# Kernel tuning notes

Hardware: AMD Instinct MI355X
Metric: run time of the kernel (lower is better)

## Reference

```python
import jax, jax.numpy as jnp
import numpy as np
import math

B, CIN, H, W = 4, 256, 64, 64
COUT = 64
K = 7  # out_kernel


def setup_inputs() -> dict:
    key = jax.random.key(0)
    ks = jax.random.split(key, 9)
    s = 0.05
    x = jax.random.normal(ks[0], (B, CIN, H, W), dtype=jnp.float32)
    Wq = jax.random.normal(ks[1], (COUT, CIN), dtype=jnp.float32) * s
    bq = jax.random.normal(ks[2], (COUT,), dtype=jnp.float32) * s
    Wk = jax.random.normal(ks[3], (COUT, CIN), dtype=jnp.float32) * s
    bk = jax.random.normal(ks[4], (COUT,), dtype=jnp.float32) * s
    Wv = jax.random.normal(ks[5], (COUT, CIN), dtype=jnp.float32) * s
    bv = jax.random.normal(ks[6], (COUT,), dtype=jnp.float32) * s
    Wout = jax.random.normal(ks[7], (COUT, COUT, K, K), dtype=jnp.float32) * s
    bout = jax.random.normal(ks[8], (COUT,), dtype=jnp.float32) * s
    return {"x": x, "Wq": Wq, "bq": bq, "Wk": Wk, "bk": bk,
            "Wv": Wv, "bv": bv, "Wout": Wout, "bout": bout}


def reference(x, Wq, bq, Wk, bk, Wv, bv, Wout, bout):
    b, c, h, w = x.shape
    C = Wq.shape[0]
    hw = h * w
    # 1x1 convs -> (b, h, w, C) channels-last
    qs = jnp.einsum('bchw,oc->bhwo', x, Wq) + bq
    ksp = jnp.einsum('bchw,oc->bhwo', x, Wk) + bk
    vs = jnp.einsum('bchw,oc->bhwo', x, Wv) + bv
    # full QK^T attention over all h*w positions
    qk = jnp.einsum('bic,bjc->bij',
                    qs.reshape(b, hw, C), ksp.reshape(b, hw, C)) / math.sqrt(float(C))
    diag = jnp.arange(hw)
    qk = qk.at[:, diag, diag].set(0.0)  # diagonal zeroed BEFORE softmax
    attn = jax.nn.softmax(qk, axis=-1).reshape(b, h, w, h, w)
    # clamped local-window indices (offsets -K//2 .. K//2)
    off = jnp.arange(K) - K // 2
    idx_h = jnp.clip(jnp.arange(h)[:, None] + off[None, :], 0, h - 1)  # (h,K)
    idx_w = jnp.clip(jnp.arange(w)[:, None] + off[None, :], 0, w - 1)  # (w,K)
    # gather attention weights at local neighborhood: (b,h,w,K,K)
    g = jnp.take_along_axis(attn, idx_h[None, :, None, :, None], axis=3)  # (b,h,w,K,w)
    g = jnp.take_along_axis(g, idx_w[None, None, :, None, :], axis=4)     # (b,h,w,K,K)
    # gather V at local neighborhood: (b,h,w,K,K,C)
    vn = vs[:, idx_h]            # (b,h,K,w,C)
    vn = vn[:, :, :, idx_w]      # (b,h,K,w,K,C)
    vn = jnp.transpose(vn, (0, 1, 3, 2, 4, 5))  # (b,h,w,K,K,C)
    # KxK stride-K conv over the (K,K) window == full contraction per pixel
    out = jnp.einsum('bhwij,bhwijc,ocij->bhwo', g, vn, Wout) + bout
    out = jax.nn.relu(out)
    return jnp.transpose(out, (0, 3, 1, 2))  # (b, C, h, w)
```

## Files before the change

### kernel.cpp

```cpp
#include <hip/hip_runtime.h>
#include <hip/hip_bf16.h>
#include <math.h>

#define BATCH 4
#define CIN   256
#define HH    64
#define WW    64
#define HW    4096
#define COUT  64
#define KK    7
#define NTAP  49
#define NSEG  16

#define QSCALE 0.18033688011112042f

typedef __attribute__((ext_vector_type(8))) short bf16x8;
typedef __attribute__((ext_vector_type(4))) float f32x4;
typedef __attribute__((ext_vector_type(4))) unsigned short u16x4;

__global__ void prep_kernel(
    const float* __restrict__ Wq, const float* __restrict__ bq,
    const float* __restrict__ Wk, const float* __restrict__ bk,
    const float* __restrict__ Wv, const float* __restrict__ bv,
    const float* __restrict__ Wout,
    __hip_bfloat16* __restrict__ Wb192, float* __restrict__ bias192,
    __hip_bfloat16* __restrict__ W2b)
{
    const int idx = blockIdx.x * 256 + threadIdx.x;
    if (idx < 192 * 256) {
        const int row = idx >> 8, c = idx & 255;
        float wsrc;
        if (row < 64)       wsrc = Wq[row * 256 + c];
        else if (row < 128) wsrc = Wk[(row - 64) * 256 + c];
        else                wsrc = Wv[(row - 128) * 256 + c];
        Wb192[idx] = __float2bfloat16(wsrc);
        if (c == 0) {
            float bsrc;
            if (row < 64)       bsrc = bq[row];
            else if (row < 128) bsrc = bk[row - 64];
            else                bsrc = bv[row - 128];
            bias192[row] = bsrc;
        }
    } else if (idx < 192 * 256 + COUT * NTAP * COUT) {
        const int j = idx - 192 * 256;
        const int o = j / (NTAP * COUT);
        const int r = j - o * (NTAP * COUT);
        const int t = r >> 6;
        const int c = r & 63;
        W2b[j] = __float2bfloat16(Wout[((size_t)o * COUT + c) * NTAP + t]);
    }
}

__global__ __launch_bounds__(256) void qkv_mfma(
    const float* __restrict__ x,
    const __hip_bfloat16* __restrict__ Wb192, const float* __restrict__ bias192,
    float* __restrict__ v,
    __hip_bfloat16* __restrict__ qh, __hip_bfloat16* __restrict__ kh)
{
    const int blk = blockIdx.x;
    const int b   = blk >> 8;
    const int p0  = (blk & 255) * 16;
    const int tid = threadIdx.x;
    const int wv  = tid >> 6;
    const int l   = tid & 63;
    const int lg  = l >> 4, lr = l & 15;

    __shared__ __attribute__((aligned(16))) __hip_bfloat16 xsh[16 * 256];

    {
        const int c0 = tid >> 2;
        const int p4 = tid & 3;
        const float4* xb4 = (const float4*)(x + ((size_t)b * CIN) * HW + p0);
#pragma unroll
        for (int it = 0; it < 4; ++it) {
            const int cc = c0 + it * 64;
            const float4 xv = xb4[(size_t)cc * (HW / 4) + p4];
            __hip_bfloat16* dst = &xsh[((cc >> 3) * 16) * 8 + (cc & 7)];
            dst[(p4 * 4 + 0) * 8] = __float2bfloat16(xv.x);
            dst[(p4 * 4 + 1) * 8] = __float2bfloat16(xv.y);
            dst[(p4 * 4 + 2) * 8] = __float2bfloat16(xv.z);
            dst[(p4 * 4 + 3) * 8] = __float2bfloat16(xv.w);
        }
    }
    __syncthreads();

    f32x4 acc0 = {0.f,0.f,0.f,0.f}, acc1 = {0.f,0.f,0.f,0.f}, acc2 = {0.f,0.f,0.f,0.f};
    const short* wb  = (const short*)Wb192;
    const short* xs  = (const short*)xsh;

#pragma unroll
    for (int s = 0; s < 8; ++s) {
        const bf16x8 af = *(const bf16x8*)(xs + (size_t)(((s * 4 + lg) * 16 + lr)) * 8);
        const bf16x8 b0 = *(const bf16x8*)(wb + (size_t)((wv * 3 + 0) * 16 + lr) * 256 + s * 32 + lg * 8);
        const bf16x8 b1 = *(const bf16x8*)(wb + (size_t)((wv * 3 + 1) * 16 + lr) * 256 + s * 32 + lg * 8);
        const bf16x8 b2 = *(const bf16x8*)(wb + (size_t)((wv * 3 + 2) * 16 + lr) * 256 + s * 32 + lg * 8);
        acc0 = __builtin_amdgcn_mfma_f32_16x16x32_bf16(af, b0, acc0, 0, 0, 0);
        acc1 = __builtin_amdgcn_mfma_f32_16x16x32_bf16(af, b1, acc1, 0, 0, 0);
        acc2 = __builtin_amdgcn_mfma_f32_16x16x32_bf16(af, b2, acc2, 0, 0, 0);
    }

    f32x4 accs[3] = {acc0, acc1, acc2};
#pragma unroll
    for (int i = 0; i < 3; ++i) {
        const int otile = wv * 3 + i;
        const int kind  = otile >> 2;
        const int o     = (otile & 3) * 16 + lr;
        const float bias = bias192[otile * 16 + lr];
#pragma unroll
        for (int j = 0; j < 4; ++j) {
            const int p = p0 + lg * 4 + j;
            const size_t addr = ((size_t)b * HW + p) * (size_t)COUT + o;
            const float val = accs[i][j] + bias;
            if (kind == 0)      { qh[addr] = __float2bfloat16(val * QSCALE); }
            else if (kind == 1) { kh[addr] = __float2bfloat16(val); }
            else                { v[addr] = val; }
        }
    }
}

__global__ __launch_bounds__(256) void qk_stats_mfma(
    const __hip_bfloat16* __restrict__ qh, const __hip_bfloat16* __restrict__ kh,
    float* __restrict__ s_part)
{
    const int blk   = blockIdx.x;
    const int b     = blk >> 8;
    const int panel = (blk >> 4) & 15;
    const int jseg  = blk & 15;
    const int tid   = threadIdx.x;
    const int w     = tid >> 6;
    const int l     = tid & 63;
    const int lg    = l >> 4;
    const int lr    = l & 15;
    const int R0    = panel * 256 + w * 64;

    const short* qb = (const short*)(qh + ((size_t)b * HW) * COUT);
    const short* kb = (const short*)(kh + ((size_t)b * HW) * COUT);

    bf16x8 a[4][2];
#pragma unroll
    for (int rt = 0; rt < 4; ++rt) {
        a[rt][0] = *(const bf16x8*)(qb + (size_t)(R0 + rt * 16 + lr) * COUT + lg * 8);
        a[rt][1] = *(const bf16x8*)(qb + (size_t)(R0 + rt * 16 + lr) * COUT + 32 + lg * 8);
    }

    float s[4][4];
#pragma unroll
    for (int rt = 0; rt < 4; ++rt)
#pragma unroll
        for (int i = 0; i < 4; ++i) s[rt][i] = 0.f;

    const int j0 = jseg * 256;
    const short* kptr = kb + (size_t)(j0 + lr) * COUT + lg * 8;

    bf16x8 p0 = *(const bf16x8*)(kptr);
    bf16x8 p1 = *(const bf16x8*)(kptr + 32);
    kptr += 16 * COUT;

    for (int it = 0; it < 16; ++it) {
        bf16x8 n0, n1;
        if (it != 15) {
            n0 = *(const bf16x8*)(kptr);
            n1 = *(const bf16x8*)(kptr + 32);
            kptr += 16 * COUT;
        }
        const int jb = j0 + it * 16;
#pragma unroll
        for (int rt = 0; rt < 4; ++rt) {
            f32x4 d = {0.f, 0.f, 0.f, 0.f};
            d = __builtin_amdgcn_mfma_f32_16x16x32_bf16(a[rt][0], p0, d, 0, 0, 0);
            d = __builtin_amdgcn_mfma_f32_16x16x32_bf16(a[rt][1], p1, d, 0, 0, 0);
            if (jb == R0 + rt * 16) {
                d.x = (lr == lg * 4 + 0) ? 0.f : d.x;
                d.y = (lr == lg * 4 + 1) ? 0.f : d.y;
                d.z = (lr == lg * 4 + 2) ? 0.f : d.z;
                d.w = (lr == lg * 4 + 3) ? 0.f : d.w;
            }
            s[rt][0] += exp2f(d.x);
            s[rt][1] += exp2f(d.y);
            s[rt][2] += exp2f(d.z);
            s[rt][3] += exp2f(d.w);
        }
        p0 = n0; p1 = n1;
    }

#pragma unroll
    for (int rt = 0; rt < 4; ++rt) {
#pragma unroll
        for (int off = 1; off < 16; off <<= 1) {
            s[rt][0] += __shfl_xor(s[rt][0], off, 64);
            s[rt][1] += __shfl_xor(s[rt][1], off, 64);
            s[rt][2] += __shfl_xor(s[rt][2], off, 64);
            s[rt][3] += __shfl_xor(s[rt][3], off, 64);
        }
        if (lr == 0) {
            float4 res = {s[rt][0], s[rt][1], s[rt][2], s[rt][3]};
            *(float4*)(s_part + (size_t)jseg * (BATCH * HW) + (size_t)b * HW +
                       R0 + rt * 16 + lg * 4) = res;
        }
    }
}

__global__ __launch_bounds__(256) void gcalc_mfma(
    const __hip_bfloat16* __restrict__ qh, const __hip_bfloat16* __restrict__ kh,
    const float* __restrict__ s_part, float* __restrict__ g)
{
    const int blk = blockIdx.x;
    const int dh  = blk % 7;
    const int bh  = blk / 7;
    const int h   = bh & 63;
    const int b   = bh >> 6;
    const int tid = threadIdx.x;
    const int wv  = tid >> 6;
    const int l   = tid & 63;
    const int lg  = l >> 4, lr = l & 15;

    const int jh = min(max(h + dh - 3, 0), HH - 1);

    __shared__ float Dsh[64][65];
    __shared__ float rsh[64];

    if (tid < 64) {
        float s = 0.f;
        const size_t base = (size_t)b * HW + h * 64 + tid;
#pragma unroll
        for (int seg = 0; seg < NSEG; ++seg)
            s += s_part[(size_t)seg * (BATCH * HW) + base];
        rsh[tid] = 1.0f / s;
    }

    const short* qb = (const short*)(qh + ((size_t)b * HW + h * 64) * COUT);
    const short* kb = (const short*)(kh + ((size_t)b * HW + jh * 64) * COUT);

    const bf16x8 a0 = *(const bf16x8*)(qb + (size_t)(wv * 16 + lr) * COUT + lg * 8);
    const bf16x8 a1 = *(const bf16x8*)(qb + (size_t)(wv * 16 + lr) * COUT + 32 + lg * 8);

#pragma unroll
    for (int ct = 0; ct < 4; ++ct) {
        const bf16x8 b0 = *(const bf16x8*)(kb + (size_t)(ct * 16 + lr) * COUT + lg * 8);
        const bf16x8 b1 = *(const bf16x8*)(kb + (size_t)(ct * 16 + lr) * COUT + 32 + lg * 8);
        f32x4 d = {0.f, 0.f, 0.f, 0.f};
        d = __builtin_amdgcn_mfma_f32_16x16x32_bf16(a0, b0, d, 0, 0, 0);
        d = __builtin_amdgcn_mfma_f32_16x16x32_bf16(a1, b1, d, 0, 0, 0);
        const int row = wv * 16 + lg * 4;
        const int col = ct * 16 + lr;
        Dsh[row + 0][col] = d.x;
        Dsh[row + 1][col] = d.y;
        Dsh[row + 2][col] = d.z;
        Dsh[row + 3][col] = d.w;
    }
    __syncthreads();

    for (int e = tid; e < 64 * 7; e += 256) {
        const int w  = e / 7;
        const int tj = e - w * 7;
        const int jw = min(max(w + tj - 3, 0), WW - 1);
        const float num = (jh == h && jw == w) ? 1.0f : exp2f(Dsh[w][jw]);
        g[((size_t)b * HW + h * 64 + w) * NTAP + dh * 7 + tj] = num * rsh[w];
    }
}

__global__ __launch_bounds__(256) void out_mfma(
    const float* __restrict__ g, const float* __restrict__ v,
    const __hip_bfloat16* __restrict__ W2b, const float* __restrict__ bout,
    float* __restrict__ out)
{
    const int blk = blockIdx.x;
    const int b   = blk >> 7;
    const int h   = (blk >> 1) & 63;
    const int w0  = (blk & 1) * 32;
    const int tid = threadIdx.x;
    const int wv  = tid >> 6;
    const int l   = tid & 63;
    const int lg  = l >> 4, lr = l & 15;

    __shared__ __attribute__((aligned(16))) __hip_bfloat16 gvsh[2][32][72];
    __shared__ float gsh[32][NTAP];

    const int row0 = b * HW + h * 64 + w0;
    for (int i = tid; i < 32 * NTAP; i += 256) {
        const int w = i / NTAP, t = i - w * NTAP;
        gsh[w][t] = g[(size_t)(row0 + w) * NTAP + t];
    }

    f32x4 acc0 = {0.f, 0.f, 0.f, 0.f};
    f32x4 acc1 = {0.f, 0.f, 0.f, 0.f};
    const float4* vb = (const float4*)(v + ((size_t)b * HW) * COUT);
    const short* wb  = (const short*)W2b + (size_t)(wv * 16 + lr) * (NTAP * COUT);

    const int fw = tid >> 4;
    const int fc4 = tid & 15;

    __syncthreads();

    for (int t = 0; t < NTAP; ++t) {
        const int dh = t / 7 - 3, dw = t - (t / 7) * 7 - 3;
        const int jh = min(max(h + dh, 0), HH - 1);
        __hip_bfloat16* dstbuf = &gvsh[t & 1][0][0];
#pragma unroll
        for (int rep = 0; rep < 2; ++rep) {
            const int w  = fw + rep * 16;
            const int jw = min(max(w0 + w + dw, 0), WW - 1);
            const float4 vvv = vb[(size_t)((jh << 6) + jw) * 16 + fc4];
            const float gg = gsh[w][t];
            u16x4 pk;
            pk.x = __builtin_bit_cast(unsigned short, __float2bfloat16(vvv.x * gg));
            pk.y = __builtin_bit_cast(unsigned short, __float2bfloat16(vvv.y * gg));
            pk.z = __builtin_bit_cast(unsigned short, __float2bfloat16(vvv.z * gg));
            pk.w = __builtin_bit_cast(unsigned short, __float2bfloat16(vvv.w * gg));
            *(u16x4*)(dstbuf + w * 72 + fc4 * 4) = pk;
        }
        const bf16x8 b0 = *(const bf16x8*)(wb + t * 64 + lg * 8);
        const bf16x8 b1 = *(const bf16x8*)(wb + t * 64 + 32 + lg * 8);
        __syncthreads();
        const short* gsrc = (const short*)&gvsh[t & 1][0][0];
        const bf16x8 a00 = *(const bf16x8*)(gsrc + (size_t)lr * 72 + lg * 8);
        const bf16x8 a01 = *(const bf16x8*)(gsrc + (size_t)lr * 72 + 32 + lg * 8);
        const bf16x8 a10 = *(const bf16x8*)(gsrc + (size_t)(16 + lr) * 72 + lg * 8);
        const bf16x8 a11 = *(const bf16x8*)(gsrc + (size_t)(16 + lr) * 72 + 32 + lg * 8);
        acc0 = __builtin_amdgcn_mfma_f32_16x16x32_bf16(a00, b0, acc0, 0, 0, 0);
        acc0 = __builtin_amdgcn_mfma_f32_16x16x32_bf16(a01, b1, acc0, 0, 0, 0);
        acc1 = __builtin_amdgcn_mfma_f32_16x16x32_bf16(a10, b0, acc1, 0, 0, 0);
        acc1 = __builtin_amdgcn_mfma_f32_16x16x32_bf16(a11, b1, acc1, 0, 0, 0);
    }

    const int o  = wv * 16 + lr;
    const float bo = bout[o];
    float* obase = out + ((size_t)(b * COUT + o) * HW) + h * 64 + w0 + lg * 4;
    float4 r0, r1;
    r0.x = fmaxf(acc0.x + bo, 0.f); r0.y = fmaxf(acc0.y + bo, 0.f);
    r0.z = fmaxf(acc0.z + bo, 0.f); r0.w = fmaxf(acc0.w + bo, 0.f);
    r1.x = fmaxf(acc1.x + bo, 0.f); r1.y = fmaxf(acc1.y + bo, 0.f);
    r1.z = fmaxf(acc1.z + bo, 0.f); r1.w = fmaxf(acc1.w + bo, 0.f);
    *(float4*)obase        = r0;
    *(float4*)(obase + 16) = r1;
}

extern "C" void kernel_launch(void* const* d_in, const int* in_sizes, int n_in,
                              void* d_out, int out_size, void* d_ws, size_t ws_size,
                              hipStream_t stream)
{
    const float* x    = (const float*)d_in[0];
    const float* Wq   = (const float*)d_in[1];
    const float* bq   = (const float*)d_in[2];
    const float* Wk   = (const float*)d_in[3];
    const float* bk   = (const float*)d_in[4];
    const float* Wv   = (const float*)d_in[5];
    const float* bv   = (const float*)d_in[6];
    const float* Wout = (const float*)d_in[7];
    const float* bout = (const float*)d_in[8];
    float* out = (float*)d_out;

    float* ws      = (float*)d_ws;
    float* v       = ws;
    float* s_part  = v + (size_t)BATCH * HW * COUT;
    float* g       = s_part + (size_t)NSEG * BATCH * HW;
    float* bias192 = g + (size_t)BATCH * HW * NTAP;
    __hip_bfloat16* qh    = (__hip_bfloat16*)(bias192 + 256);
    __hip_bfloat16* kh    = qh + (size_t)BATCH * HW * COUT;
    __hip_bfloat16* W2b   = kh + (size_t)BATCH * HW * COUT;
    __hip_bfloat16* Wb192 = W2b + (size_t)COUT * NTAP * COUT;

    prep_kernel<<<(192 * 256 + COUT * NTAP * COUT + 255) / 256, 256, 0, stream>>>(
        Wq, bq, Wk, bk, Wv, bv, Wout, Wb192, bias192, W2b);
    qkv_mfma<<<BATCH * (HW / 16), 256, 0, stream>>>(x, Wb192, bias192, v, qh, kh);
    qk_stats_mfma<<<BATCH * 16 * NSEG, 256, 0, stream>>>(qh, kh, s_part);
    gcalc_mfma<<<BATCH * HH * 7, 256, 0, stream>>>(qh, kh, s_part, g);
    out_mfma<<<512, 256, 0, stream>>>(g, v, W2b, bout, out);
}
```

Before: 183.5 us.

## Split out_mfma taps across waves and reduce partial accumulators in LDS

Restructures the output-conv kernel so that each of the four waves handles a disjoint subset of the 49 taps for all 64 output channels, instead of every wave covering all taps for 16 channels. Each wave now builds its A fragments (g-scaled V in bf16) directly in registers from global memory. This removes the per-tap shared-memory staging buffer and the per-tap __syncthreads. The partial accumulators are then summed across waves through an LDS buffer before bias and ReLU. In exchange the kernel needs more accumulator registers, more redundant global loads of V (each lane loads 8 floats per slice), and extra LDS for the final reduction.

```diff
diff --git a/kernel.cpp b/kernel.cpp
--- a/kernel.cpp
+++ b/kernel.cpp
@@ -273,66 +273,91 @@
     const int l   = tid & 63;
     const int lg  = l >> 4, lr = l & 15;
 
-    __shared__ __attribute__((aligned(16))) __hip_bfloat16 gvsh[2][32][72];
     __shared__ float gsh[32][NTAP];
+    __shared__ __attribute__((aligned(16))) float accsh[4][64][36];
 
     const int row0 = b * HW + h * 64 + w0;
     for (int i = tid; i < 32 * NTAP; i += 256) {
         const int w = i / NTAP, t = i - w * NTAP;
         gsh[w][t] = g[(size_t)(row0 + w) * NTAP + t];
     }
-
-    f32x4 acc0 = {0.f, 0.f, 0.f, 0.f};
-    f32x4 acc1 = {0.f, 0.f, 0.f, 0.f};
-    const float4* vb = (const float4*)(v + ((size_t)b * HW) * COUT);
-    const short* wb  = (const short*)W2b + (size_t)(wv * 16 + lr) * (NTAP * COUT);
-
-    const int fw = tid >> 4;
-    const int fc4 = tid & 15;
-
     __syncthreads();
 
-    for (int t = 0; t < NTAP; ++t) {
+    f32x4 acc[2][4];
+#pragma unroll
+    for (int rep = 0; rep < 2; ++rep)
+#pragma unroll
+        for (int ot = 0; ot < 4; ++ot)
+            acc[rep][ot] = (f32x4){0.f, 0.f, 0.f, 0.f};
+
+    const float* vb = v + ((size_t)b * HW) * COUT;
+    const short* wbase = (const short*)W2b;
+
+    for (int t = wv; t < NTAP; t += 4) {
         const int dh = t / 7 - 3, dw = t - (t / 7) * 7 - 3;
         const int jh = min(max(h + dh, 0), HH - 1);
-        __hip_bfloat16* dstbuf = &gvsh[t & 1][0][0];
+
+        bf16x8 A[2][2];
 #pragma unroll
         for (int rep = 0; rep < 2; ++rep) {
-            const int w  = fw + rep * 16;
+            const int w  = rep * 16 + lr;
             const int jw = min(max(w0 + w + dw, 0), WW - 1);
-            const float4 vvv = vb[(size_t)((jh << 6) + jw) * 16 + fc4];
             const float gg = gsh[w][t];
-            u16x4 pk;
-            pk.x = __builtin_bit_cast(unsigned short, __float2bfloat16(vvv.x * gg));
-            pk.y = __builtin_bit_cast(unsigned short, __float2bfloat16(vvv.y * gg));
-            pk.z = __builtin_bit_cast(unsigned short, __float2bfloat16(vvv.z * gg));
-            pk.w = __builtin_bit_cast(unsigned short, __float2bfloat16(vvv.w * gg));
-            *(u16x4*)(dstbuf + w * 72 + fc4 * 4) = pk;
-        }
-        const bf16x8 b0 = *(const bf16x8*)(wb + t * 64 + lg * 8);
-        const bf16x8 b1 = *(const bf16x8*)(wb + t * 64 + 32 + lg * 8);
-        __syncthreads();
-        const short* gsrc = (const short*)&gvsh[t & 1][0][0];
-        const bf16x8 a00 = *(const bf16x8*)(gsrc + (size_t)lr * 72 + lg * 8);
-        const bf16x8 a01 = *(const bf16x8*)(gsrc + (size_t)lr * 72 + 32 + lg * 8);
-        const bf16x8 a10 = *(const bf16x8*)(gsrc + (size_t)(16 + lr) * 72 + lg * 8);
-        const bf16x8 a11 = *(const bf16x8*)(gsrc + (size_t)(16 + lr) * 72 + 32 + lg * 8);
-        acc0 = __builtin_amdgcn_mfma_f32_16x16x32_bf16(a00, b0, acc0, 0, 0, 0);
-        acc0 = __builtin_amdgcn_mfma_f32_16x16x32_bf16(a01, b1, acc0, 0, 0, 0);
-        acc1 = __builtin_amdgcn_mfma_f32_16x16x32_bf16(a10, b0, acc1, 0, 0, 0);
-        acc1 = __builtin_amdgcn_mfma_f32_16x16x32_bf16(a11, b1, acc1, 0, 0, 0);
-    }
-
-    const int o  = wv * 16 + lr;
+            const float* vr = vb + (size_t)((jh << 6) + jw) * COUT;
+#pragma unroll
+            for (int sl = 0; sl < 2; ++sl) {
+                const float4 lo = *(const float4*)(vr + sl * 32 + lg * 8);
+                const float4 hi = *(const float4*)(vr + sl * 32 + lg * 8 + 4);
+                bf16x8 av;
+                av[0] = (short)__builtin_bit_cast(unsigned short, __float2bfloat16(lo.x * gg));
+                av[1] = (short)__builtin_bit_cast(unsigned short, __float2bfloat16(lo.y * gg));
+                av[2] = (short)__builtin_bit_cast(unsigned short, __float2bfloat16(lo.z * gg));
+                av[3] = (short)__builtin_bit_cast(unsigned short, __float2bfloat16(lo.w * gg));
+                av[4] = (short)__builtin_bit_cast(unsigned short, __float2bfloat16(hi.x * gg));
+                av[5] = (short)__builtin_bit_cast(unsigned short, __float2bfloat16(hi.y * gg));
+                av[6] = (short)__builtin_bit_cast(unsigned short, __float2bfloat16(hi.z * gg));
+                av[7] = (short)__builtin_bit_cast(unsigned short, __float2bfloat16(hi.w * gg));
+                A[rep][sl] = av;
+            }
+        }
+
+#pragma unroll
+        for (int ot = 0; ot < 4; ++ot) {
+            const short* wrow = wbase + (size_t)(ot * 16 + lr) * (NTAP * COUT) + t * 64;
+            const bf16x8 B0 = *(const bf16x8*)(wrow + lg * 8);
+            const bf16x8 B1 = *(const bf16x8*)(wrow + 32 + lg * 8);
+            acc[0][ot] = __builtin_amdgcn_mfma_f32_16x16x32_bf16(A[0][0], B0, acc[0][ot], 0, 0, 0);
+            acc[0][ot] = __builtin_amdgcn_mfma_f32_16x16x32_bf16(A[0][1], B1, acc[0][ot], 0, 0, 0);
+            acc[1][ot] = __builtin_amdgcn_mfma_f32_16x16x32_bf16(A[1][0], B0, acc[1][ot], 0, 0, 0);
+            acc[1][ot] = __builtin_amdgcn_mfma_f32_16x16x32_bf16(A[1][1], B1, acc[1][ot], 0, 0, 0);
+        }
+    }
+
+#pragma unroll
+    for (int rep = 0; rep < 2; ++rep)
+#pragma unroll
+        for (int ot = 0; ot < 4; ++ot)
+            *(f32x4*)&accsh[wv][ot * 16 + lr][rep * 16 + lg * 4] = acc[rep][ot];
+    __syncthreads();
+
+    const int o  = tid >> 2;
+    const int pr = (tid & 3) * 8;
+    float4 sA = {0.f, 0.f, 0.f, 0.f}, sB = {0.f, 0.f, 0.f, 0.f};
+#pragma unroll
+    for (int w = 0; w < 4; ++w) {
+        const float4 a = *(const float4*)&accsh[w][o][pr];
+        const float4 c = *(const float4*)&accsh[w][o][pr + 4];
+        sA.x += a.x; sA.y += a.y; sA.z += a.z; sA.w += a.w;
+        sB.x += c.x; sB.y += c.y; sB.z += c.z; sB.w += c.w;
+    }
     const float bo = bout[o];
-    float* obase = out + ((size_t)(b * COUT + o) * HW) + h * 64 + w0 + lg * 4;
-    float4 r0, r1;
-    r0.x = fmaxf(acc0.x + bo, 0.f); r0.y = fmaxf(acc0.y + bo, 0.f);
-    r0.z = fmaxf(acc0.z + bo, 0.f); r0.w = fmaxf(acc0.w + bo, 0.f);
-    r1.x = fmaxf(acc1.x + bo, 0.f); r1.y = fmaxf(acc1.y + bo, 0.f);
-    r1.z = fmaxf(acc1.z + bo, 0.f); r1.w = fmaxf(acc1.w + bo, 0.f);
-    *(float4*)obase        = r0;
-    *(float4*)(obase + 16) = r1;
+    sA.x = fmaxf(sA.x + bo, 0.f); sA.y = fmaxf(sA.y + bo, 0.f);
+    sA.z = fmaxf(sA.z + bo, 0.f); sA.w = fmaxf(sA.w + bo, 0.f);
+    sB.x = fmaxf(sB.x + bo, 0.f); sB.y = fmaxf(sB.y + bo, 0.f);
+    sB.z = fmaxf(sB.z + bo, 0.f); sB.w = fmaxf(sB.w + bo, 0.f);
+    float* obase = out + ((size_t)(b * COUT + o) * HW) + h * 64 + w0 + pr;
+    *(float4*)obase       = sA;
+    *(float4*)(obase + 4) = sB;
 }
 
 extern "C" void kernel_launch(void* const* d_in, const int* in_sizes, int n_in,
```

After: 193.4 us. 1.05x slower.

## Prefetch next-tap V and weights in out_mfma and repack Wout for coalescing

Applied to the files above, without the earlier changes.

The out_mfma loop now issues the global loads of V and the bf16 output weights for tap t+1 before the barrier and MFMAs of tap t, so memory latency overlaps compute. The Wout repack is changed to a tap-major, k-block-interleaved layout so that each lane's 8-element B fragment load is contiguous and neighbouring lanes read adjacent addresses. This adds register pressure from the in-flight prefetch registers. It only affects the final kernel, which is one of five.

```diff
diff --git a/kernel.cpp b/kernel.cpp
--- a/kernel.cpp
+++ b/kernel.cpp
@@ -24,7 +24,7 @@
     const float* __restrict__ Wv, const float* __restrict__ bv,
     const float* __restrict__ Wout,
     __hip_bfloat16* __restrict__ Wb192, float* __restrict__ bias192,
-    __hip_bfloat16* __restrict__ W2b)
+    __hip_bfloat16* __restrict__ W2p)
 {
     const int idx = blockIdx.x * 256 + threadIdx.x;
     if (idx < 192 * 256) {
@@ -41,13 +41,14 @@
             else                bsrc = bv[row - 128];
             bias192[row] = bsrc;
         }
-    } else if (idx < 192 * 256 + COUT * NTAP * COUT) {
-        const int j = idx - 192 * 256;
-        const int o = j / (NTAP * COUT);
-        const int r = j - o * (NTAP * COUT);
-        const int t = r >> 6;
-        const int c = r & 63;
-        W2b[j] = __float2bfloat16(Wout[((size_t)o * COUT + c) * NTAP + t]);
+    } else if (idx < 192 * 256 + NTAP * 8 * COUT * 8) {
+        const int j  = idx - 192 * 256;
+        const int e  = j & 7;
+        const int o  = (j >> 3) & 63;
+        const int kb = (j >> 9) & 7;
+        const int t  = j >> 12;
+        const int c  = kb * 8 + e;
+        W2p[j] = __float2bfloat16(Wout[((size_t)o * COUT + c) * NTAP + t]);
     }
 }
 
@@ -261,7 +262,7 @@
 
 __global__ __launch_bounds__(256) void out_mfma(
     const float* __restrict__ g, const float* __restrict__ v,
-    const __hip_bfloat16* __restrict__ W2b, const float* __restrict__ bout,
+    const __hip_bfloat16* __restrict__ W2p, const float* __restrict__ bout,
     float* __restrict__ out)
 {
     const int blk = blockIdx.x;
@@ -282,45 +283,68 @@
         gsh[w][t] = g[(size_t)(row0 + w) * NTAP + t];
     }
 
+    const int fw  = tid >> 4;
+    const int fc4 = tid & 15;
+    const float* vb = v + ((size_t)b * HW) * COUT;
+
+    auto vaddr = [&](int t, int rep) -> const float4* {
+        const int dh = t / 7 - 3, dw = t - (t / 7) * 7 - 3;
+        const int jh = min(max(h + dh, 0), HH - 1);
+        const int jw = min(max(w0 + fw + rep * 16 + dw, 0), WW - 1);
+        return (const float4*)(vb + (size_t)((jh << 6) + jw) * COUT) + fc4;
+    };
+
+    const short* wp = (const short*)W2p;
+    auto baddr = [&](int t, int sl) -> const bf16x8* {
+        return (const bf16x8*)(wp + (size_t)(((t * 8 + sl * 4 + lg) << 6) + wv * 16 + lr) * 8);
+    };
+
+    float4 vv0 = *vaddr(0, 0);
+    float4 vv1 = *vaddr(0, 1);
+    bf16x8 Bc0 = *baddr(0, 0);
+    bf16x8 Bc1 = *baddr(0, 1);
+    __syncthreads();
+
     f32x4 acc0 = {0.f, 0.f, 0.f, 0.f};
     f32x4 acc1 = {0.f, 0.f, 0.f, 0.f};
-    const float4* vb = (const float4*)(v + ((size_t)b * HW) * COUT);
-    const short* wb  = (const short*)W2b + (size_t)(wv * 16 + lr) * (NTAP * COUT);
-
-    const int fw = tid >> 4;
-    const int fc4 = tid & 15;
-
-    __syncthreads();
 
     for (int t = 0; t < NTAP; ++t) {
-        const int dh = t / 7 - 3, dw = t - (t / 7) * 7 - 3;
-        const int jh = min(max(h + dh, 0), HH - 1);
-        __hip_bfloat16* dstbuf = &gvsh[t & 1][0][0];
-#pragma unroll
-        for (int rep = 0; rep < 2; ++rep) {
-            const int w  = fw + rep * 16;
-            const int jw = min(max(w0 + w + dw, 0), WW - 1);
-            const float4 vvv = vb[(size_t)((jh << 6) + jw) * 16 + fc4];
-            const float gg = gsh[w][t];
-            u16x4 pk;
-            pk.x = __builtin_bit_cast(unsigned short, __float2bfloat16(vvv.x * gg));
-            pk.y = __builtin_bit_cast(unsigned short, __float2bfloat16(vvv.y * gg));
-            pk.z = __builtin_bit_cast(unsigned short, __float2bfloat16(vvv.z * gg));
-            pk.w = __builtin_bit_cast(unsigned short, __float2bfloat16(vvv.w * gg));
-            *(u16x4*)(dstbuf + w * 72 + fc4 * 4) = pk;
-        }
-        const bf16x8 b0 = *(const bf16x8*)(wb + t * 64 + lg * 8);
-        const bf16x8 b1 = *(const bf16x8*)(wb + t * 64 + 32 + lg * 8);
+        {
+            const float g0 = gsh[fw][t], g1 = gsh[fw + 16][t];
+            u16x4 pk0, pk1;
+            pk0.x = __builtin_bit_cast(unsigned short, __float2bfloat16(vv0.x * g0));
+            pk0.y = __builtin_bit_cast(unsigned short, __float2bfloat16(vv0.y * g0));
+            pk0.z = __builtin_bit_cast(unsigned short, __float2bfloat16(vv0.z * g0));
+            pk0.w = __builtin_bit_cast(unsigned short, __float2bfloat16(vv0.w * g0));
+            pk1.x = __builtin_bit_cast(unsigned short, __float2bfloat16(vv1.x * g1));
+            pk1.y = __builtin_bit_cast(unsigned short, __float2bfloat16(vv1.y * g1));
+            pk1.z = __builtin_bit_cast(unsigned short, __float2bfloat16(vv1.z * g1));
+            pk1.w = __builtin_bit_cast(unsigned short, __float2bfloat16(vv1.w * g1));
+            *(u16x4*)(&gvsh[t & 1][fw][fc4 * 4])      = pk0;
+            *(u16x4*)(&gvsh[t & 1][fw + 16][fc4 * 4]) = pk1;
+        }
+
+        float4 vn0, vn1;
+        bf16x8 Bn0, Bn1;
+        if (t != NTAP - 1) {
+            vn0 = *vaddr(t + 1, 0);
+            vn1 = *vaddr(t + 1, 1);
+            Bn0 = *baddr(t + 1, 0);
+            Bn1 = *baddr(t + 1, 1);
+        }
+
         __syncthreads();
         const short* gsrc = (const short*)&gvsh[t & 1][0][0];
         const bf16x8 a00 = *(const bf16x8*)(gsrc + (size_t)lr * 72 + lg * 8);
         const bf16x8 a01 = *(const bf16x8*)(gsrc + (size_t)lr * 72 + 32 + lg * 8);
         const bf16x8 a10 = *(const bf16x8*)(gsrc + (size_t)(16 + lr) * 72 + lg * 8);
         const bf16x8 a11 = *(const bf16x8*)(gsrc + (size_t)(16 + lr) * 72 + 32 + lg * 8);
-        acc0 = __builtin_amdgcn_mfma_f32_16x16x32_bf16(a00, b0, acc0, 0, 0, 0);
-        acc0 = __builtin_amdgcn_mfma_f32_16x16x32_bf16(a01, b1, acc0, 0, 0, 0);
-        acc1 = __builtin_amdgcn_mfma_f32_16x16x32_bf16(a10, b0, acc1, 0, 0, 0);
-        acc1 = __builtin_amdgcn_mfma_f32_16x16x32_bf16(a11, b1, acc1, 0, 0, 0);
+        acc0 = __builtin_amdgcn_mfma_f32_16x16x32_bf16(a00, Bc0, acc0, 0, 0, 0);
+        acc0 = __builtin_amdgcn_mfma_f32_16x16x32_bf16(a01, Bc1, acc0, 0, 0, 0);
+        acc1 = __builtin_amdgcn_mfma_f32_16x16x32_bf16(a10, Bc0, acc1, 0, 0, 0);
+        acc1 = __builtin_amdgcn_mfma_f32_16x16x32_bf16(a11, Bc1, acc1, 0, 0, 0);
+
+        vv0 = vn0; vv1 = vn1; Bc0 = Bn0; Bc1 = Bn1;
     }
 
     const int o  = wv * 16 + lr;
@@ -357,13 +381,13 @@
     float* bias192 = g + (size_t)BATCH * HW * NTAP;
     __hip_bfloat16* qh    = (__hip_bfloat16*)(bias192 + 256);
     __hip_bfloat16* kh    = qh + (size_t)BATCH * HW * COUT;
-    __hip_bfloat16* W2b   = kh + (size_t)BATCH * HW * COUT;
-    __hip_bfloat16* Wb192 = W2b + (size_t)COUT * NTAP * COUT;
-
-    prep_kernel<<<(192 * 256 + COUT * NTAP * COUT + 255) / 256, 256, 0, stream>>>(
-        Wq, bq, Wk, bk, Wv, bv, Wout, Wb192, bias192, W2b);
+    __hip_bfloat16* W2p   = kh + (size_t)BATCH * HW * COUT;
+    __hip_bfloat16* Wb192 = W2p + (size_t)NTAP * 8 * COUT * 8;
+
+    prep_kernel<<<(192 * 256 + NTAP * 8 * COUT * 8 + 255) / 256, 256, 0, stream>>>(
+        Wq, bq, Wk, bk, Wv, bv, Wout, Wb192, bias192, W2p);
     qkv_mfma<<<BATCH * (HW / 16), 256, 0, stream>>>(x, Wb192, bias192, v, qh, kh);
     qk_stats_mfma<<<BATCH * 16 * NSEG, 256, 0, stream>>>(qh, kh, s_part);
     gcalc_mfma<<<BATCH * HH * 7, 256, 0, stream>>>(qh, kh, s_part, g);
-    out_mfma<<<512, 256, 0, stream>>>(g, v, W2b, bout, out);
-}
+    out_mfma<<<512, 256, 0, stream>>>(g, v, W2p, bout, out);
+}
```

After: 168.6 us. -8.1%, faster.
